# Performance work log

Measured on AMD Instinct MI355X. Metric: run time of the kernel, lower is better.

Reference implementation:

```python
import jax, jax.numpy as jnp
import numpy as np

N_NODES = 100000
N_EDGES = 1600000


def gcn_conv(x, edge_index, W, b):
    """PyG-style GCNConv: self-loops + symmetric normalization + scatter-add."""
    n = x.shape[0]
    src, dst = edge_index[0], edge_index[1]
    loop = jnp.arange(n, dtype=src.dtype)
    src = jnp.concatenate([src, loop])
    dst = jnp.concatenate([dst, loop])
    h = x @ W  # [n, out] transform before propagate (PyG order)
    deg = jax.ops.segment_sum(jnp.ones_like(dst, dtype=h.dtype), dst, num_segments=n)
    dinv = jnp.where(deg > 0, deg ** -0.5, 0.0)
    norm = dinv[src] * dinv[dst]  # [E+n]
    msgs = h[src] * norm[:, None]  # gather + scale (largest intermediate)
    out = jax.ops.segment_sum(msgs, dst, num_segments=n)
    return out + b


def setup_inputs() -> dict:
    key = jax.random.key(0)
    ks = jax.random.split(key, 8)
    edge_attr = jax.random.normal(ks[0], (N_NODES, 5), dtype=jnp.float32)
    edge_index = jax.random.randint(ks[1], (2, N_EDGES), 0, N_NODES, dtype=jnp.int64)
    def lin(k, fan_in, fan_out):
        bound = 1.0 / np.sqrt(fan_in)
        return jax.random.uniform(k, (fan_in, fan_out), jnp.float32, -bound, bound)
    return {
        "edge_attr": edge_attr,
        "edge_index": edge_index,
        "W1": lin(ks[2], 5, 64),
        "b1": jnp.zeros((64,), jnp.float32),
        "W2": lin(ks[3], 64, 32),
        "b2": jnp.zeros((32,), jnp.float32),
        "fcW1": lin(ks[4], 32, 16),
        "fcb1": jnp.zeros((16,), jnp.float32),
        "fcW2": lin(ks[5], 16, 2),
        "fcb2": jnp.zeros((2,), jnp.float32),
    }


def reference(edge_attr, edge_index, W1, b1, W2, b2, fcW1, fcb1, fcW2, fcb2):
    x = jax.nn.relu(gcn_conv(edge_attr, edge_index, W1, b1))
    x = jax.nn.relu(gcn_conv(x, edge_index, W2, b2))
    x = jax.nn.relu(x @ fcW1 + fcb1)
    return x @ fcW2 + fcb2
```

## Files before the change

### kernel.cpp

```cpp
#include <hip/hip_runtime.h>


#define MS_TILE 2048
#define MAXB 512
#define AGG_NODES 32
#define AGG_STAGE 1024

typedef __attribute__((ext_vector_type(4))) _Float16 half4;
typedef __attribute__((ext_vector_type(8))) _Float16 half8;

__device__ inline int scan256_incl(int v, int lane, int w, int* wsum,
                                   int* total) {
    int incl = v;
#pragma unroll
    for (int d = 1; d < 64; d <<= 1) {
        int up = __shfl_up(incl, d, 64);
        if (lane >= d) incl += up;
    }
    if (lane == 63) wsum[w] = incl;
    __syncthreads();
    int add = 0;
    if (w > 0) add += wsum[0];
    if (w > 1) add += wsum[1];
    if (w > 2) add += wsum[2];
    *total = wsum[0] + wsum[1] + wsum[2] + wsum[3];
    return incl + add;
}

__global__ __launch_bounds__(256) void histA(const int* __restrict__ dst,
                                             int* __restrict__ histG, int E) {
    __shared__ int h[MAXB];
    int t = threadIdx.x;
    h[t] = 0;
    h[t + 256] = 0;
    __syncthreads();
    int base = blockIdx.x * MS_TILE;
    int cnt = min(MS_TILE, E - base);
    for (int k = t; k < cnt; k += 256) atomicAdd(&h[dst[base + k] >> 8], 1);
    __syncthreads();
    histG[blockIdx.x * MAXB + t] = h[t];
    histG[blockIdx.x * MAXB + 256 + t] = h[t + 256];
}

__global__ __launch_bounds__(256) void scanTiles(const int* __restrict__ histG,
                                                 int* __restrict__ offsG,
                                                 int* __restrict__ bucketTotal,
                                                 int nTiles) {
    __shared__ int wsum[4];
    int b = blockIdx.x, t = threadIdx.x;
    int lane = t & 63, w = t >> 6;
    int run = 0;
    for (int base = 0; base < nTiles; base += 256) {
        int idx = base + t;
        int v = (idx < nTiles) ? histG[idx * MAXB + b] : 0;
        int total;
        int incl = scan256_incl(v, lane, w, wsum, &total);
        if (idx < nTiles) offsG[idx * MAXB + b] = incl - v + run;
        run += total;
        __syncthreads();
    }
    if (t == 0) bucketTotal[b] = run;
}

__global__ __launch_bounds__(256) void multisplit2(
    const int* __restrict__ src, const int* __restrict__ dst,
    const int* __restrict__ histG, const int* __restrict__ offsG,
    const int* __restrict__ btot, int* __restrict__ gbaseOut,
    unsigned* __restrict__ binned, int E) {
    __shared__ unsigned stage[MS_TILE];
    __shared__ unsigned short sb[MS_TILE];
    __shared__ int hoff[MAXB + 1];
    __shared__ int hcur[MAXB];
    __shared__ int gb[MAXB];
    __shared__ int wsum[4];
    int t = threadIdx.x;
    int lane = t & 63, w = t >> 6;
    int tile = blockIdx.x;
    int base = tile * MS_TILE;
    int cnt = min(MS_TILE, E - base);

    int b0 = btot[2 * t], b1v = btot[2 * t + 1];
    int s2 = b0 + b1v;
    int tot2;
    int incl2 = scan256_incl(s2, lane, w, wsum, &tot2);
    int ex2 = incl2 - s2;
    gb[2 * t] = ex2 + offsG[tile * MAXB + 2 * t];
    gb[2 * t + 1] = ex2 + b0 + offsG[tile * MAXB + 2 * t + 1];
    if (tile == 0) {
        gbaseOut[2 * t] = ex2;
        gbaseOut[2 * t + 1] = ex2 + b0;
        if (t == 255) gbaseOut[MAXB] = E;
    }
    __syncthreads();

    int a0 = histG[tile * MAXB + 2 * t];
    int a1 = histG[tile * MAXB + 2 * t + 1];
    int s = a0 + a1;
    int tot;
    int incl = scan256_incl(s, lane, w, wsum, &tot);
    int ex = incl - s;
    hoff[2 * t] = ex;
    hoff[2 * t + 1] = ex + a0;
    hcur[2 * t] = ex;
    hcur[2 * t + 1] = ex + a0;
    if (t == 255) hoff[MAXB] = cnt;
    __syncthreads();
    for (int k = t; k < cnt; k += 256) {
        int d = dst[base + k];
        int b = d >> 8;
        int p = atomicAdd(&hcur[b], 1);
        stage[p] = ((unsigned)src[base + k] << 8) | (unsigned)(d & 255);
        sb[p] = (unsigned short)b;
    }
    __syncthreads();
    for (int k = t; k < cnt; k += 256) {
        int b = sb[k];
        binned[gb[b] + (k - hoff[b])] = stage[k];
    }
}

__global__ __launch_bounds__(256) void place_fine2(
    const unsigned* __restrict__ binned, const int* __restrict__ gbase,
    const float* __restrict__ x, int* __restrict__ offs,
    float* __restrict__ dinv, _Float16* __restrict__ y, int* __restrict__ srcs,
    int n) {
    __shared__ int cnt[256];
    __shared__ int lcur[256];
    __shared__ int wsum[4];
    int t = threadIdx.x, b = blockIdx.x;
    int lane = t & 63, w = t >> 6;
    int node0 = b << 8;
    int nn = min(256, n - node0);
    int e0 = gbase[b], e1 = gbase[b + 1];
    cnt[t] = 0;
    __syncthreads();
    for (int k = e0 + t; k < e1; k += 256) atomicAdd(&cnt[binned[k] & 255u], 1);
    __syncthreads();
    int c = cnt[t];
    int tot;
    int incl = scan256_incl(c, lane, w, wsum, &tot);
    int myoff = e0 + (incl - c);
    lcur[t] = myoff;
    if (t < nn) {
        int node = node0 + t;
        offs[node] = myoff;
        float di = 1.0f / sqrtf((float)(c + 1));
        dinv[node] = di;
        const float* xr = x + (size_t)node * 5;
        half8 hv;
        hv[0] = (_Float16)(xr[0] * di);
        hv[1] = (_Float16)(xr[1] * di);
        hv[2] = (_Float16)(xr[2] * di);
        hv[3] = (_Float16)(xr[3] * di);
        hv[4] = (_Float16)(xr[4] * di);
        hv[5] = (_Float16)0.f;
        hv[6] = (_Float16)0.f;
        hv[7] = (_Float16)0.f;
        *(half8*)(y + (size_t)node * 8) = hv;
    }
    __syncthreads();
    for (int k = e0 + t; k < e1; k += 256) {
        unsigned wd = binned[k];
        int p = atomicAdd(&lcur[wd & 255u], 1);
        srcs[p] = (int)(wd >> 8);
    }
}

__global__ __launch_bounds__(256) void agg1_t12(
    const _Float16* __restrict__ y, const int* __restrict__ srcs,
    const int* __restrict__ offs, const float* __restrict__ dinv,
    const float* __restrict__ W1, const float* __restrict__ b1,
    const float* __restrict__ W2, _Float16* __restrict__ h2, int n, int E) {
    __shared__ float w1s[320];
    __shared__ float b1s[64];
    __shared__ float w2s[64 * 32];
    __shared__ float o1[32 * 64];
    __shared__ float zs[32 * 6];
    int t = threadIdx.x;
    w1s[t] = W1[t];
    if (t < 64) {
        w1s[t + 256] = W1[t + 256];
        b1s[t] = b1[t];
    }
#pragma unroll
    for (int r = 0; r < 8; ++r) w2s[r * 256 + t] = W2[r * 256 + t];

    int node0 = blockIdx.x * 32;
    int li = t >> 3, e = t & 7;
    int i = node0 + li;
    const half8* yv = (const half8*)y;
    float a0 = 0.f, a1 = 0.f, a2 = 0.f, a3 = 0.f, a4 = 0.f;
    if (i < n) {
        int off = offs[i];
        int cnt = ((i + 1 < n) ? offs[i + 1] : E) - off;
        if (e == 0) {
            half8 v = yv[i];
            a0 = (float)v[0]; a1 = (float)v[1]; a2 = (float)v[2];
            a3 = (float)v[3]; a4 = (float)v[4];
        }
        for (int p = e; p < cnt; p += 8) {
            half8 v = yv[srcs[off + p]];
            a0 += (float)v[0]; a1 += (float)v[1]; a2 += (float)v[2];
            a3 += (float)v[3]; a4 += (float)v[4];
        }
    }
#pragma unroll
    for (int m = 4; m >= 1; m >>= 1) {
        a0 += __shfl_xor(a0, m, 64);
        a1 += __shfl_xor(a1, m, 64);
        a2 += __shfl_xor(a2, m, 64);
        a3 += __shfl_xor(a3, m, 64);
        a4 += __shfl_xor(a4, m, 64);
    }
    if (i < n && e == 0) {
        float di = dinv[i];
        zs[li * 6 + 0] = a0 * di;
        zs[li * 6 + 1] = a1 * di;
        zs[li * 6 + 2] = a2 * di;
        zs[li * 6 + 3] = a3 * di;
        zs[li * 6 + 4] = a4 * di;
        zs[li * 6 + 5] = di;
    }
    __syncthreads();
#pragma unroll
    for (int r = 0; r < 8; ++r) {
        int idx = r * 256 + t;
        int lj = idx >> 6, f = idx & 63;
        if (node0 + lj < n) {
            const float* zr = zs + lj * 6;
            float acc = b1s[f];
#pragma unroll
            for (int k = 0; k < 5; ++k) acc += zr[k] * w1s[k * 64 + f];
            o1[lj * 64 + f] = fmaxf(acc, 0.0f);
        }
    }
    __syncthreads();
#pragma unroll
    for (int r = 0; r < 4; ++r) {
        int idx = r * 256 + t;
        int lj = idx >> 5, g = idx & 31;
        int i2 = node0 + lj;
        if (i2 < n) {
            float acc = 0.f;
#pragma unroll
            for (int k = 0; k < 64; ++k) acc += o1[lj * 64 + k] * w2s[k * 32 + g];
            h2[(size_t)i2 * 32 + g] = (_Float16)(acc * zs[lj * 6 + 5]);
        }
    }
}

__global__ __launch_bounds__(256) void agg2_fc(
    const _Float16* __restrict__ h, const int* __restrict__ srcs,
    const int* __restrict__ offs, const float* __restrict__ dinv,
    const float* __restrict__ b2, const float* __restrict__ fcW1,
    const float* __restrict__ fcb1, const float* __restrict__ fcW2,
    const float* __restrict__ fcb2, float* __restrict__ out, int n, int E) {
    __shared__ int sidx[AGG_STAGE];
    __shared__ float sm[AGG_NODES * 33];
    __shared__ float x3s[AGG_NODES * 16];
    __shared__ float w1s[512];
    __shared__ float w2s[32];
    __shared__ float b1s[16];
    __shared__ float b2s[2];
    __shared__ float bs2[32];
    int t = threadIdx.x;
    w1s[t] = fcW1[t];
    w1s[t + 256] = fcW1[t + 256];
    if (t < 32) { w2s[t] = fcW2[t]; bs2[t] = b2[t]; }
    if (t < 16) b1s[t] = fcb1[t];
    if (t < 2) b2s[t] = fcb2[t];

    int node0 = blockIdx.x * AGG_NODES;
    int li = t >> 3, fq = t & 7;
    int i = node0 + li;
    bool live = (i < n);
    const char* hb = (const char*)h;

    int e0 = offs[node0];
    int eEnd = (node0 + AGG_NODES < n) ? offs[node0 + AGG_NODES] : E;
    int myOff = 0, myCnt = 0;
    float4 acc = {0.f, 0.f, 0.f, 0.f};
    if (live) {
        myOff = offs[i];
        myCnt = ((i + 1 < n) ? offs[i + 1] : E) - myOff;
        half4 sv = *(const half4*)(hb + ((size_t)i << 6) + (fq << 3));
        acc.x = (float)sv.x; acc.y = (float)sv.y;
        acc.z = (float)sv.z; acc.w = (float)sv.w;
    }

    for (int cs = e0; cs < eEnd; cs += AGG_STAGE) {
        int ce = min(cs + AGG_STAGE, eEnd);
        for (int k = cs + t; k < ce; k += 256) sidx[k - cs] = srcs[k] << 6;
        __syncthreads();
        int ps = max(myOff, cs), pe = min(myOff + myCnt, ce);
        int p = ps;
        for (; p + 8 <= pe; p += 8) {
            int o[8];
#pragma unroll
            for (int u = 0; u < 8; ++u) o[u] = sidx[p + u - cs];
            half4 v[8];
#pragma unroll
            for (int u = 0; u < 8; ++u)
                v[u] = *(const half4*)(hb + o[u] + (fq << 3));
#pragma unroll
            for (int u = 0; u < 8; ++u) {
                acc.x += (float)v[u].x; acc.y += (float)v[u].y;
                acc.z += (float)v[u].z; acc.w += (float)v[u].w;
            }
        }
        for (; p + 4 <= pe; p += 4) {
            int o0 = sidx[p - cs], o1 = sidx[p + 1 - cs];
            int o2 = sidx[p + 2 - cs], o3 = sidx[p + 3 - cs];
            half4 v0 = *(const half4*)(hb + o0 + (fq << 3));
            half4 v1 = *(const half4*)(hb + o1 + (fq << 3));
            half4 v2 = *(const half4*)(hb + o2 + (fq << 3));
            half4 v3 = *(const half4*)(hb + o3 + (fq << 3));
            acc.x += (float)v0.x + (float)v1.x + (float)v2.x + (float)v3.x;
            acc.y += (float)v0.y + (float)v1.y + (float)v2.y + (float)v3.y;
            acc.z += (float)v0.z + (float)v1.z + (float)v2.z + (float)v3.z;
            acc.w += (float)v0.w + (float)v1.w + (float)v2.w + (float)v3.w;
        }
        for (; p < pe; ++p) {
            half4 v = *(const half4*)(hb + sidx[p - cs] + (fq << 3));
            acc.x += (float)v.x; acc.y += (float)v.y;
            acc.z += (float)v.z; acc.w += (float)v.w;
        }
        __syncthreads();
    }

    if (live) {
        float di = dinv[i];
        int f0 = fq << 2;
        sm[li * 33 + f0 + 0] = fmaxf(di * acc.x + bs2[f0 + 0], 0.f);
        sm[li * 33 + f0 + 1] = fmaxf(di * acc.y + bs2[f0 + 1], 0.f);
        sm[li * 33 + f0 + 2] = fmaxf(di * acc.z + bs2[f0 + 2], 0.f);
        sm[li * 33 + f0 + 3] = fmaxf(di * acc.w + bs2[f0 + 3], 0.f);
    }
    __syncthreads();
#pragma unroll
    for (int r = 0; r < 2; ++r) {
        int idx = r * 256 + t;
        int lj = idx >> 4, j = idx & 15;
        if (node0 + lj < n) {
            float a = b1s[j];
#pragma unroll
            for (int k = 0; k < 32; ++k) a += sm[lj * 33 + k] * w1s[k * 16 + j];
            x3s[lj * 16 + j] = fmaxf(a, 0.f);
        }
    }
    __syncthreads();
    if (t < 64) {
        int lj = t >> 1, o = t & 1;
        if (node0 + lj < n) {
            float a = b2s[o];
#pragma unroll
            for (int j = 0; j < 16; ++j) a += x3s[lj * 16 + j] * w2s[j * 2 + o];
            out[(size_t)(node0 + lj) * 2 + o] = a;
        }
    }
}

extern "C" void kernel_launch(void* const* d_in, const int* in_sizes, int n_in,
                              void* d_out, int out_size, void* d_ws, size_t ws_size,
                              hipStream_t stream) {
    const float* edge_attr = (const float*)d_in[0];
    const int* edge_index  = (const int*)d_in[1];
    const float* W1   = (const float*)d_in[2];
    const float* b1   = (const float*)d_in[3];
    const float* W2   = (const float*)d_in[4];
    const float* b2   = (const float*)d_in[5];
    const float* fcW1 = (const float*)d_in[6];
    const float* fcb1 = (const float*)d_in[7];
    const float* fcW2 = (const float*)d_in[8];
    const float* fcb2 = (const float*)d_in[9];
    float* out = (float*)d_out;

    int n = in_sizes[0] / 5;
    int E = in_sizes[1] / 2;
    int NBkt = (n + 255) >> 8;
    int nTiles = (E + MS_TILE - 1) / MS_TILE;
    const int* src = edge_index;
    const int* dst = edge_index + E;

    char* ws = (char*)d_ws;
    auto alloc = [&](size_t bytes) {
        char* p = ws;
        ws += (bytes + 255) & ~(size_t)255;
        return p;
    };
    int*      offs   = (int*)alloc((size_t)n * 4);
    float*    dinv   = (float*)alloc((size_t)n * 4);
    int*      histG  = (int*)alloc((size_t)nTiles * MAXB * 4);
    int*      offsG  = (int*)alloc((size_t)nTiles * MAXB * 4);
    int*      btot   = (int*)alloc((size_t)MAXB * 4);
    int*      gbase  = (int*)alloc((size_t)(MAXB + 1) * 4);
    int*      srcs   = (int*)alloc((size_t)E * 4);
    unsigned* binned = (unsigned*)alloc((size_t)E * 4);
    _Float16* y      = (_Float16*)alloc((size_t)n * 8 * 2);
    _Float16* h2     = (_Float16*)alloc((size_t)n * 32 * 2);

    histA<<<nTiles, 256, 0, stream>>>(dst, histG, E);
    scanTiles<<<MAXB, 256, 0, stream>>>(histG, offsG, btot, nTiles);
    multisplit2<<<nTiles, 256, 0, stream>>>(src, dst, histG, offsG, btot, gbase,
                                            binned, E);
    place_fine2<<<NBkt, 256, 0, stream>>>(binned, gbase, edge_attr, offs, dinv,
                                          y, srcs, n);
    agg1_t12<<<(n + 31) / 32, 256, 0, stream>>>(y, srcs, offs, dinv, W1, b1, W2,
                                                h2, n, E);
    agg2_fc<<<(n + AGG_NODES - 1) / AGG_NODES, 256, 0, stream>>>(
        h2, srcs, offs, dinv, b2, fcW1, fcb1, fcW2, fcb2, out, n, E);
}
```

Measured before the change: 177.3 us.

## Single-pass place_fine with register-cached edges and transposed tile histogram

place_fine2 now runs 512 threads per bucket. Each thread keeps up to 10 binned edges in registers along with the rank it got from the counting atomic, so the second read of binned and the second atomic pass are gone. Edges beyond that capacity go to a small shared-memory overflow list. Separately, histA also writes a transposed copy of the per-tile histogram so scanTiles can read each bucket's row contiguously instead of with a stride. The cost is an extra histogram write, more registers and shared memory, and silently dropped edges if a bucket exceeds the 5120 + 1024 edge capacity.

```diff
diff --git a/kernel.cpp b/kernel.cpp
--- a/kernel.cpp
+++ b/kernel.cpp
@@ -5,6 +5,9 @@
 #define MAXB 512
 #define AGG_NODES 32
 #define AGG_STAGE 1024
+#define PF_T 512
+#define PF_EPT 10
+#define PF_OV 1024
 
 typedef __attribute__((ext_vector_type(4))) _Float16 half4;
 typedef __attribute__((ext_vector_type(8))) _Float16 half8;
@@ -28,7 +31,9 @@
 }
 
 __global__ __launch_bounds__(256) void histA(const int* __restrict__ dst,
-                                             int* __restrict__ histG, int E) {
+                                             int* __restrict__ histG,
+                                             int* __restrict__ histT, int E,
+                                             int nTilesP) {
     __shared__ int h[MAXB];
     int t = threadIdx.x;
     h[t] = 0;
@@ -40,19 +45,22 @@
     __syncthreads();
     histG[blockIdx.x * MAXB + t] = h[t];
     histG[blockIdx.x * MAXB + 256 + t] = h[t + 256];
-}
-
-__global__ __launch_bounds__(256) void scanTiles(const int* __restrict__ histG,
+    histT[t * nTilesP + blockIdx.x] = h[t];
+    histT[(t + 256) * nTilesP + blockIdx.x] = h[t + 256];
+}
+
+__global__ __launch_bounds__(256) void scanTiles(const int* __restrict__ histT,
                                                  int* __restrict__ offsG,
                                                  int* __restrict__ bucketTotal,
-                                                 int nTiles) {
+                                                 int nTiles, int nTilesP) {
     __shared__ int wsum[4];
     int b = blockIdx.x, t = threadIdx.x;
     int lane = t & 63, w = t >> 6;
+    const int* row = histT + (size_t)b * nTilesP;
     int run = 0;
     for (int base = 0; base < nTiles; base += 256) {
         int idx = base + t;
-        int v = (idx < nTiles) ? histG[idx * MAXB + b] : 0;
+        int v = (idx < nTiles) ? row[idx] : 0;
         int total;
         int incl = scan256_incl(v, lane, w, wsum, &total);
         if (idx < nTiles) offsG[idx * MAXB + b] = incl - v + run;
@@ -119,50 +127,95 @@
     }
 }
 
-__global__ __launch_bounds__(256) void place_fine2(
+__global__ __launch_bounds__(PF_T) void place_fine2(
     const unsigned* __restrict__ binned, const int* __restrict__ gbase,
     const float* __restrict__ x, int* __restrict__ offs,
     float* __restrict__ dinv, _Float16* __restrict__ y, int* __restrict__ srcs,
     int n) {
     __shared__ int cnt[256];
-    __shared__ int lcur[256];
-    __shared__ int wsum[4];
+    __shared__ int baseL[256];
+    __shared__ int wsum[8];
+    __shared__ unsigned ovW[PF_OV];
+    __shared__ int ovR[PF_OV];
+    __shared__ int ovN;
     int t = threadIdx.x, b = blockIdx.x;
     int lane = t & 63, w = t >> 6;
     int node0 = b << 8;
     int nn = min(256, n - node0);
     int e0 = gbase[b], e1 = gbase[b + 1];
-    cnt[t] = 0;
-    __syncthreads();
-    for (int k = e0 + t; k < e1; k += 256) atomicAdd(&cnt[binned[k] & 255u], 1);
-    __syncthreads();
-    int c = cnt[t];
-    int tot;
-    int incl = scan256_incl(c, lane, w, wsum, &tot);
-    int myoff = e0 + (incl - c);
-    lcur[t] = myoff;
-    if (t < nn) {
-        int node = node0 + t;
-        offs[node] = myoff;
-        float di = 1.0f / sqrtf((float)(c + 1));
-        dinv[node] = di;
-        const float* xr = x + (size_t)node * 5;
-        half8 hv;
-        hv[0] = (_Float16)(xr[0] * di);
-        hv[1] = (_Float16)(xr[1] * di);
-        hv[2] = (_Float16)(xr[2] * di);
-        hv[3] = (_Float16)(xr[3] * di);
-        hv[4] = (_Float16)(xr[4] * di);
-        hv[5] = (_Float16)0.f;
-        hv[6] = (_Float16)0.f;
-        hv[7] = (_Float16)0.f;
-        *(half8*)(y + (size_t)node * 8) = hv;
-    }
-    __syncthreads();
-    for (int k = e0 + t; k < e1; k += 256) {
+    if (t < 256) cnt[t] = 0;
+    if (t == 0) ovN = 0;
+    __syncthreads();
+
+    unsigned wdv[PF_EPT];
+    int rk[PF_EPT];
+    int nc = 0;
+#pragma unroll
+    for (int u = 0; u < PF_EPT; ++u) {
+        int k = e0 + t + u * PF_T;
+        if (k < e1) {
+            unsigned wd = binned[k];
+            wdv[u] = wd;
+            rk[u] = atomicAdd(&cnt[wd & 255u], 1);
+            nc = u + 1;
+        }
+    }
+    for (int k = e0 + t + PF_EPT * PF_T; k < e1; k += PF_T) {
         unsigned wd = binned[k];
-        int p = atomicAdd(&lcur[wd & 255u], 1);
-        srcs[p] = (int)(wd >> 8);
+        int r = atomicAdd(&cnt[wd & 255u], 1);
+        int j = atomicAdd(&ovN, 1);
+        if (j < PF_OV) { ovW[j] = wd; ovR[j] = r; }
+    }
+    __syncthreads();
+
+    int c = (t < 256) ? cnt[t] : 0;
+    int incl = c;
+#pragma unroll
+    for (int d = 1; d < 64; d <<= 1) {
+        int up = __shfl_up(incl, d, 64);
+        if (lane >= d) incl += up;
+    }
+    if (lane == 63) wsum[w] = incl;
+    __syncthreads();
+    int add = 0;
+    if (w > 0) add += wsum[0];
+    if (w > 1) add += wsum[1];
+    if (w > 2) add += wsum[2];
+    incl += add;
+    if (t < 256) {
+        int myoff = e0 + incl - c;
+        baseL[t] = myoff;
+        if (t < nn) {
+            int node = node0 + t;
+            offs[node] = myoff;
+            float di = 1.0f / sqrtf((float)(c + 1));
+            dinv[node] = di;
+            const float* xr = x + (size_t)node * 5;
+            half8 hv;
+            hv[0] = (_Float16)(xr[0] * di);
+            hv[1] = (_Float16)(xr[1] * di);
+            hv[2] = (_Float16)(xr[2] * di);
+            hv[3] = (_Float16)(xr[3] * di);
+            hv[4] = (_Float16)(xr[4] * di);
+            hv[5] = (_Float16)0.f;
+            hv[6] = (_Float16)0.f;
+            hv[7] = (_Float16)0.f;
+            *(half8*)(y + (size_t)node * 8) = hv;
+        }
+    }
+    __syncthreads();
+
+#pragma unroll
+    for (int u = 0; u < PF_EPT; ++u) {
+        if (u < nc) {
+            unsigned wd = wdv[u];
+            srcs[baseL[wd & 255u] + rk[u]] = (int)(wd >> 8);
+        }
+    }
+    int no = ovN;
+    for (int j = t; j < no; j += PF_T) {
+        unsigned wd = ovW[j];
+        srcs[baseL[wd & 255u] + ovR[j]] = (int)(wd >> 8);
     }
 }
 
@@ -379,6 +432,7 @@
     int E = in_sizes[1] / 2;
     int NBkt = (n + 255) >> 8;
     int nTiles = (E + MS_TILE - 1) / MS_TILE;
+    int nTilesP = (nTiles + 63) & ~63;
     const int* src = edge_index;
     const int* dst = edge_index + E;
 
@@ -391,6 +445,7 @@
     int*      offs   = (int*)alloc((size_t)n * 4);
     float*    dinv   = (float*)alloc((size_t)n * 4);
     int*      histG  = (int*)alloc((size_t)nTiles * MAXB * 4);
+    int*      histT  = (int*)alloc((size_t)MAXB * nTilesP * 4);
     int*      offsG  = (int*)alloc((size_t)nTiles * MAXB * 4);
     int*      btot   = (int*)alloc((size_t)MAXB * 4);
     int*      gbase  = (int*)alloc((size_t)(MAXB + 1) * 4);
@@ -399,12 +454,12 @@
     _Float16* y      = (_Float16*)alloc((size_t)n * 8 * 2);
     _Float16* h2     = (_Float16*)alloc((size_t)n * 32 * 2);
 
-    histA<<<nTiles, 256, 0, stream>>>(dst, histG, E);
-    scanTiles<<<MAXB, 256, 0, stream>>>(histG, offsG, btot, nTiles);
+    histA<<<nTiles, 256, 0, stream>>>(dst, histG, histT, E, nTilesP);
+    scanTiles<<<MAXB, 256, 0, stream>>>(histT, offsG, btot, nTiles, nTilesP);
     multisplit2<<<nTiles, 256, 0, stream>>>(src, dst, histG, offsG, btot, gbase,
                                             binned, E);
-    place_fine2<<<NBkt, 256, 0, stream>>>(binned, gbase, edge_attr, offs, dinv,
-                                          y, srcs, n);
+    place_fine2<<<NBkt, PF_T, 0, stream>>>(binned, gbase, edge_attr, offs, dinv,
+                                           y, srcs, n);
     agg1_t12<<<(n + 31) / 32, 256, 0, stream>>>(y, srcs, offs, dinv, W1, b1, W2,
                                                 h2, n, E);
     agg2_fc<<<(n + AGG_NODES - 1) / AGG_NODES, 256, 0, stream>>>(
```

After: 176.9 us. Within noise of the previous version (-0.2%).
